# Optimization experiments

Hardware: AMD Instinct MI355X
Metric: run time of the kernel (lower is better)

The kernel has to match this reference:

```python
import jax, jax.numpy as jnp
import numpy as np

B, N, E, H = 4, 4096, 1024, 16
D = E // H


def setup_inputs() -> dict:
    key = jax.random.key(0)
    ks = jax.random.split(key, 8)
    s = 1.0 / np.sqrt(E)
    x = jax.random.normal(ks[0], (B, N, E), dtype=jnp.float32)
    # binary multiplicative sparsity pattern over the head-head score matrix
    sparsity_pattern = jax.random.randint(ks[1], (H, H), 0, 2).astype(jnp.float32)
    Wq = jax.random.normal(ks[2], (E, E), dtype=jnp.float32) * s
    bq = jax.random.normal(ks[3], (E,), dtype=jnp.float32) * s
    Wk = jax.random.normal(ks[4], (E, E), dtype=jnp.float32) * s
    bk = jax.random.normal(ks[5], (E,), dtype=jnp.float32) * s
    Wv = jax.random.normal(ks[6], (E, E), dtype=jnp.float32) * s
    bv = jax.random.normal(ks[7], (E,), dtype=jnp.float32) * s
    return {"x": x, "sparsity_pattern": sparsity_pattern,
            "Wq": Wq, "bq": bq, "Wk": Wk, "bk": bk, "Wv": Wv, "bv": bv}


def reference(x, sparsity_pattern, Wq, bq, Wk, bk, Wv, bv):
    b, n, e = x.shape
    # torch Linear: y = x @ W.T + b
    q = (x @ Wq.T + bq).reshape(b, n, H, D)
    k = (x @ Wk.T + bk).reshape(b, n, H, D)
    v = (x @ Wv.T + bv).reshape(b, n, H, D)
    # torch.matmul over last two dims of [B,N,H,D]: scores are [B,N,H,H]
    scores = jnp.einsum('bnhd,bngd->bnhg', q, k) * sparsity_pattern
    attn = jax.nn.softmax(scores, axis=-1)
    out = jnp.einsum('bnhg,bngd->bnhd', attn, v).reshape(b, n, e)
    return out
```

## Files before the change

kernel.cpp:

```cpp
#include <hip/hip_runtime.h>
#include <hip/hip_bf16.h>

#define M_   16384
#define K_   1024
#define NQKV 3072

typedef _Float16 f16x4 __attribute__((ext_vector_type(4)));
typedef _Float16 f16x8 __attribute__((ext_vector_type(8)));
typedef float    f32x4 __attribute__((ext_vector_type(4)));

__global__ __launch_bounds__(256) void cvt_f32_f16(const float* __restrict__ in,
                                                   _Float16* __restrict__ o, int n4) {
  int i = blockIdx.x * blockDim.x + threadIdx.x;
  const int stride = gridDim.x * blockDim.x;
  for (; i < n4; i += stride) {
    float4 v = ((const float4*)in)[i];
    f16x4 h; h[0] = (_Float16)v.x; h[1] = (_Float16)v.y;
    h[2] = (_Float16)v.z; h[3] = (_Float16)v.w;
    *(f16x4*)&o[(size_t)i * 4] = h;
  }
}

__global__ __launch_bounds__(256) void cvt3_f32_f16(
    const float* __restrict__ a, const float* __restrict__ b,
    const float* __restrict__ c, _Float16* __restrict__ o, int n4each) {
  const float* src = (blockIdx.y == 0) ? a : (blockIdx.y == 1) ? b : c;
  _Float16* dst = o + (size_t)blockIdx.y * n4each * 4;
  int i = blockIdx.x * blockDim.x + threadIdx.x;
  const int stride = gridDim.x * blockDim.x;
  for (; i < n4each; i += stride) {
    float4 v = ((const float4*)src)[i];
    f16x4 h; h[0] = (_Float16)v.x; h[1] = (_Float16)v.y;
    h[2] = (_Float16)v.z; h[3] = (_Float16)v.w;
    *(f16x4*)&dst[(size_t)i * 4] = h;
  }
}

__global__ __launch_bounds__(512, 2) void gemm_qkv(
    const _Float16* __restrict__ xh, const _Float16* __restrict__ wh,
    const float* __restrict__ bq, const float* __restrict__ bk,
    const float* __restrict__ bv, _Float16* __restrict__ qkv)
{
  __shared__ __align__(16) _Float16 As[2][256 * 64];
  __shared__ __align__(16) _Float16 Bs[2][256 * 64];

  const int tid  = threadIdx.x;
  const int ln   = tid & 63;
  const int w    = tid >> 6;
  const int wm2  = w >> 2;
  const int wn4  = w & 3;
  const int lcol = ln & 15, quad = ln >> 4;

  const int bid = blockIdx.x;
  const int swz = (bid & 7) * 96 + (bid >> 3);
  const int m0 = (swz / 12) * 256;
  const int n0 = (swz % 12) * 256;

  f32x4 acc[8][4];
#pragma unroll
  for (int i = 0; i < 8; ++i)
#pragma unroll
    for (int j = 0; j < 4; ++j) acc[i][j] = f32x4{0.f, 0.f, 0.f, 0.f};

  f16x8 a0[4][2], a1[4][2], b0[2][2], b1[2][2];

#define STAGE_A(BUF, KT, X)                                                    \
  { _Pragma("unroll")                                                          \
    for (int j = 0; j < 2; ++j) {                                              \
      const int c   = j * 512 + tid;                                           \
      const int rr  = c >> 3;                                                  \
      const int r   = (X) * 64 + (rr & 63) + ((rr >> 6) << 7);                 \
      const int cb  = (c & 7) ^ (r & 7);                                       \
      const int rr0 = j * 64 + w * 8;                                          \
      const int r0  = (X) * 64 + (rr0 & 63) + ((rr0 >> 6) << 7);               \
      __builtin_amdgcn_global_load_lds(                                        \
          (const __attribute__((address_space(1))) void*)(                     \
              xh + (size_t)(m0 + r) * K_ + (KT) * 64 + cb * 8),                \
          (__attribute__((address_space(3))) void*)(&As[BUF][r0 * 64]),        \
          16, 0, 0);                                                           \
    } }

#define STAGE_B(BUF, KT, Y)                                                    \
  { _Pragma("unroll")                                                          \
    for (int j = 0; j < 2; ++j) {                                              \
      const int c   = j * 512 + tid;                                           \
      const int rr  = c >> 3;                                                  \
      const int r   = ((rr >> 5) << 6) + (Y) * 32 + (rr & 31);                 \
      const int cb  = (c & 7) ^ (r & 7);                                       \
      const int rr0 = j * 64 + w * 8;                                          \
      const int r0  = ((rr0 >> 5) << 6) + (Y) * 32 + (rr0 & 31);               \
      __builtin_amdgcn_global_load_lds(                                        \
          (const __attribute__((address_space(1))) void*)(                     \
              wh + (size_t)(n0 + r) * K_ + (KT) * 64 + cb * 8),                \
          (__attribute__((address_space(3))) void*)(&Bs[BUF][r0 * 64]),        \
          16, 0, 0);                                                           \
    } }

#define RDA(DST, BUF, MH, KB)                                                  \
  _Pragma("unroll")                                                            \
  for (int mi = 0; mi < 4; ++mi) {                                             \
    const int ar = wm2 * 128 + (MH) * 64 + mi * 16 + lcol;                     \
    const int sw = ar & 7;                                                     \
    DST[mi][KB] = *(const f16x8*)&As[BUF][ar * 64 + (((KB)*4 + quad) ^ sw) * 8]; \
  }

#define RDB(DST, BUF, NH, KB)                                                  \
  _Pragma("unroll")                                                            \
  for (int ni = 0; ni < 2; ++ni) {                                             \
    const int br = wn4 * 64 + (NH) * 32 + ni * 16 + lcol;                      \
    const int sw = br & 7;                                                     \
    DST[ni][KB] = *(const f16x8*)&Bs[BUF][br * 64 + (((KB)*4 + quad) ^ sw) * 8]; \
  }

#define MFMA8(AARR, BARR, MH, NH, KB)                                          \
  __builtin_amdgcn_s_setprio(1);                                               \
  _Pragma("unroll")                                                            \
  for (int mi = 0; mi < 4; ++mi)                                               \
    _Pragma("unroll")                                                          \
    for (int ni = 0; ni < 2; ++ni)                                             \
      acc[(MH) * 4 + mi][(NH) * 2 + ni] =                                      \
          __builtin_amdgcn_mfma_f32_16x16x32_f16(                              \
              AARR[mi][KB], BARR[ni][KB], acc[(MH) * 4 + mi][(NH) * 2 + ni],   \
              0, 0, 0);                                                        \
  __builtin_amdgcn_s_setprio(0);

#define SB()    __builtin_amdgcn_sched_barrier(0)
#define BAR()   { __builtin_amdgcn_s_barrier(); SB(); }
#define LGKM(N) { asm volatile("s_waitcnt lgkmcnt(" #N ")" ::: "memory"); SB(); }
#define VM6()   asm volatile("s_waitcnt vmcnt(6)" ::: "memory")
#define VM0()   asm volatile("s_waitcnt vmcnt(0)" ::: "memory")

#define KTILE(BUF, STG1, STG2, STG3, STG4, WAIT4)                              \
  {                                               \
    RDB(b0, BUF, 0, 0); RDA(a0, BUF, 0, 0); SB();                              \
    RDB(b0, BUF, 0, 1); RDA(a0, BUF, 0, 1); SB();                              \
    STG1;                                                                      \
    BAR(); LGKM(6);  MFMA8(a0, b0, 0, 0, 0);                                   \
           LGKM(0);  MFMA8(a0, b0, 0, 0, 1); BAR();                            \
                                                        \
    RDA(a1, BUF, 1, 0); SB(); RDA(a1, BUF, 1, 1); SB();                        \
    STG2;                                                                      \
    BAR(); LGKM(4);  MFMA8(a1, b0, 1, 0, 0);                                   \
           LGKM(0);  MFMA8(a1, b0, 1, 0, 1); BAR();                            \
                                                        \
    RDB(b1, BUF, 1, 0); SB(); RDB(b1, BUF, 1, 1); SB();                        \
    STG3;                                                                      \
    BAR(); LGKM(2);  MFMA8(a1, b1, 1, 1, 0);                                   \
           LGKM(0);  MFMA8(a1, b1, 1, 1, 1); BAR();                            \
                                                 \
    STG4; WAIT4;                                                               \
    BAR();           MFMA8(a0, b1, 0, 1, 0);                                   \
                     MFMA8(a0, b1, 0, 1, 1); BAR();                            \
  }

  STAGE_A(0, 0, 0); STAGE_B(0, 0, 0); STAGE_A(0, 0, 1); STAGE_B(0, 0, 1);
  STAGE_B(1, 1, 0); STAGE_A(1, 1, 1); STAGE_B(1, 1, 1);
  VM6(); BAR();

#pragma unroll 1
  for (int it = 0; it < 7; ++it) {
    const int kt = it * 2;
    KTILE(0, STAGE_A(1, kt + 1, 0), STAGE_B(0, kt + 2, 0),
             STAGE_A(0, kt + 2, 1), STAGE_B(0, kt + 2, 1), VM6());
    KTILE(1, STAGE_A(0, kt + 2, 0), STAGE_B(1, kt + 3, 0),
             STAGE_A(1, kt + 3, 1), STAGE_B(1, kt + 3, 1), VM6());
  }
  KTILE(0, STAGE_A(1, 15, 0), , , , VM0());
  KTILE(1, , , , , );

#pragma unroll
  for (int nh = 0; nh < 4; ++nh) {
    const int col = n0 + wn4 * 64 + nh * 16 + lcol;
    const int seg = col >> 10, cs = col & 1023;
    const float bi = ((seg == 0) ? bq : (seg == 1) ? bk : bv)[cs];
#pragma unroll
    for (int mi = 0; mi < 8; ++mi) {
      const int r0 = m0 + wm2 * 128 + mi * 16 + quad * 4;
#pragma unroll
      for (int r = 0; r < 4; ++r)
        qkv[(size_t)(r0 + r) * 3072 + col] = (_Float16)(acc[mi][nh][r] + bi);
    }
  }
#undef STAGE_A
#undef STAGE_B
#undef RDA
#undef RDB
#undef MFMA8
#undef SB
#undef BAR
#undef LGKM
#undef VM6
#undef VM0
#undef KTILE
}

__global__ __launch_bounds__(256) void attn_kernel(
    const _Float16* __restrict__ qkv,
    const float* __restrict__ pat,
    float* __restrict__ out)
{
  __shared__ __align__(16) _Float16 Ps[4][16 * 24];
  __shared__ __align__(16) _Float16 Vt[4][64 * 24];

  const int tid  = threadIdx.x;
  const int ln   = tid & 63;
  const int wv   = tid >> 6;
  const int lcol = ln & 15, quad = ln >> 4;
  const int t    = blockIdx.x * 4 + wv;

  const _Float16* qg = qkv + (size_t)t * 3072;
  const _Float16* kg = qg + 1024;
  const _Float16* vg = qg + 2048;

  f16x8 vc[2];
  vc[0] = *(const f16x8*)(vg + ((ln >> 3)    ) * 64 + (ln & 7) * 8);
  vc[1] = *(const f16x8*)(vg + ((ln >> 3) + 8) * 64 + (ln & 7) * 8);
  f16x8 aq0 = *(const f16x8*)(qg + lcol * 64 + quad * 8);
  f16x8 aq1 = *(const f16x8*)(qg + lcol * 64 + 32 + quad * 8);
  f16x8 bk0 = *(const f16x8*)(kg + lcol * 64 + quad * 8);
  f16x8 bk1 = *(const f16x8*)(kg + lcol * 64 + 32 + quad * 8);
  float p4[4];
#pragma unroll
  for (int r = 0; r < 4; r++) p4[r] = pat[(quad * 4 + r) * 16 + lcol];

#pragma unroll
  for (int i = 0; i < 2; i++) {
    const int g = (ln >> 3) + i * 8, c = (ln & 7) * 8;
#pragma unroll
    for (int j = 0; j < 8; j++) Vt[wv][(c + j) * 24 + g] = vc[i][j];
  }

  f32x4 s = {0.f, 0.f, 0.f, 0.f};
  s = __builtin_amdgcn_mfma_f32_16x16x32_f16(aq0, bk0, s, 0, 0, 0);
  s = __builtin_amdgcn_mfma_f32_16x16x32_f16(aq1, bk1, s, 0, 0, 0);

#pragma unroll
  for (int r = 0; r < 4; r++) {
    const float sv = s[r] * p4[r];
    float m = sv;
#pragma unroll
    for (int msk = 1; msk < 16; msk <<= 1) m = fmaxf(m, __shfl_xor(m, msk, 64));
    const float e = __expf(sv - m);
    float su = e;
#pragma unroll
    for (int msk = 1; msk < 16; msk <<= 1) su += __shfl_xor(su, msk, 64);
    Ps[wv][(quad * 4 + r) * 24 + lcol] = (_Float16)(e / su);
  }

  f16x4 ap = *(const f16x4*)&Ps[wv][lcol * 24 + quad * 4];

  f32x4 o[4];
#pragma unroll
  for (int dt = 0; dt < 4; dt++) {
    f16x4 bvf = *(const f16x4*)&Vt[wv][(dt * 16 + lcol) * 24 + quad * 4];
    f32x4 z = {0.f, 0.f, 0.f, 0.f};
    o[dt] = __builtin_amdgcn_mfma_f32_16x16x16f16(ap, bvf, z, 0, 0, 0);
  }

  float* op = out + (size_t)t * 1024;
#pragma unroll
  for (int dt = 0; dt < 4; dt++)
#pragma unroll
    for (int r = 0; r < 4; r++)
      op[(quad * 4 + r) * 64 + dt * 16 + lcol] = o[dt][r];
}

extern "C" void kernel_launch(void* const* d_in, const int* in_sizes, int n_in,
                              void* d_out, int out_size, void* d_ws, size_t ws_size,
                              hipStream_t stream) {
  const float* x   = (const float*)d_in[0];
  const float* pat = (const float*)d_in[1];
  const float* Wq  = (const float*)d_in[2];
  const float* bq  = (const float*)d_in[3];
  const float* Wk  = (const float*)d_in[4];
  const float* bk  = (const float*)d_in[5];
  const float* Wv  = (const float*)d_in[6];
  const float* bv  = (const float*)d_in[7];

  _Float16* qkvh = (_Float16*)d_ws;
  _Float16* xh   = qkvh + (size_t)50331648;
  _Float16* wh   = qkvh + (size_t)67108864;

  cvt_f32_f16<<<4096, 256, 0, stream>>>(x, xh, 4194304);
  cvt3_f32_f16<<<dim3(256, 3), 256, 0, stream>>>(Wq, Wk, Wv, wh, 262144);

  gemm_qkv<<<768, 512, 0, stream>>>(xh, wh, bq, bk, bv, qkvh);
  attn_kernel<<<M_ / 4, 256, 0, stream>>>(qkvh, pat, (float*)d_out);
}
```

Baseline: 271.9 us.

## Restructure QKV GEMM K-loop into two-phase pipeline with register prefetch

Rewrites the K-tile schedule of the fused QKV projection GEMM. Each tile is now two phases with one barrier each, where there were four barrier-bracketed quadrants. The next tile's whole A/B stage is issued at the start of each tile, and the next tile's a0/b0 fragments are prefetched into registers (b0 ping-pongs between b0e/b0o) while the current MFMAs run. The aim is fewer barriers and better overlap of LDS reads with MFMA work. The cost is more live registers and a shallower global prefetch depth: it now runs one tile ahead and waits for vmcnt(0) each tile, so global latency may be less well hidden.

```diff
diff --git a/kernel.cpp b/kernel.cpp
--- a/kernel.cpp
+++ b/kernel.cpp
@@ -62,7 +62,7 @@
 #pragma unroll
     for (int j = 0; j < 4; ++j) acc[i][j] = f32x4{0.f, 0.f, 0.f, 0.f};
 
-  f16x8 a0[4][2], a1[4][2], b0[2][2], b1[2][2];
+  f16x8 a0[4][2], a1[4][2], b0e[2][2], b0o[2][2], b1[2][2];
 
 #define STAGE_A(BUF, KT, X)                                                    \
   { _Pragma("unroll")                                                          \
@@ -96,77 +96,79 @@
           16, 0, 0);                                                           \
     } }
 
-#define RDA(DST, BUF, MH, KB)                                                  \
+#define RDA(DST, BUF, MH)                                                      \
   _Pragma("unroll")                                                            \
   for (int mi = 0; mi < 4; ++mi) {                                             \
     const int ar = wm2 * 128 + (MH) * 64 + mi * 16 + lcol;                     \
     const int sw = ar & 7;                                                     \
-    DST[mi][KB] = *(const f16x8*)&As[BUF][ar * 64 + (((KB)*4 + quad) ^ sw) * 8]; \
-  }
-
-#define RDB(DST, BUF, NH, KB)                                                  \
+    DST[mi][0] = *(const f16x8*)&As[BUF][ar * 64 + ((quad    ) ^ sw) * 8];     \
+    DST[mi][1] = *(const f16x8*)&As[BUF][ar * 64 + ((quad + 4) ^ sw) * 8];     \
+  }
+
+#define RDB(DST, BUF, NH)                                                      \
   _Pragma("unroll")                                                            \
   for (int ni = 0; ni < 2; ++ni) {                                             \
     const int br = wn4 * 64 + (NH) * 32 + ni * 16 + lcol;                      \
     const int sw = br & 7;                                                     \
-    DST[ni][KB] = *(const f16x8*)&Bs[BUF][br * 64 + (((KB)*4 + quad) ^ sw) * 8]; \
-  }
-
-#define MFMA8(AARR, BARR, MH, NH, KB)                                          \
+    DST[ni][0] = *(const f16x8*)&Bs[BUF][br * 64 + ((quad    ) ^ sw) * 8];     \
+    DST[ni][1] = *(const f16x8*)&Bs[BUF][br * 64 + ((quad + 4) ^ sw) * 8];     \
+  }
+
+#define MFMA16(AARR, BARR, MH, NH)                                             \
   __builtin_amdgcn_s_setprio(1);                                               \
   _Pragma("unroll")                                                            \
-  for (int mi = 0; mi < 4; ++mi)                                               \
+  for (int kb = 0; kb < 2; ++kb)                                               \
     _Pragma("unroll")                                                          \
-    for (int ni = 0; ni < 2; ++ni)                                             \
-      acc[(MH) * 4 + mi][(NH) * 2 + ni] =                                      \
-          __builtin_amdgcn_mfma_f32_16x16x32_f16(                              \
-              AARR[mi][KB], BARR[ni][KB], acc[(MH) * 4 + mi][(NH) * 2 + ni],   \
-              0, 0, 0);                                                        \
+    for (int mi = 0; mi < 4; ++mi)                                             \
+      _Pragma("unroll")                                                        \
+      for (int ni = 0; ni < 2; ++ni)                                           \
+        acc[(MH) * 4 + mi][(NH) * 2 + ni] =                                    \
+            __builtin_amdgcn_mfma_f32_16x16x32_f16(                            \
+                AARR[mi][kb], BARR[ni][kb], acc[(MH) * 4 + mi][(NH) * 2 + ni], \
+                0, 0, 0);                                                      \
   __builtin_amdgcn_s_setprio(0);
 
 #define SB()    __builtin_amdgcn_sched_barrier(0)
 #define BAR()   { __builtin_amdgcn_s_barrier(); SB(); }
 #define LGKM(N) { asm volatile("s_waitcnt lgkmcnt(" #N ")" ::: "memory"); SB(); }
-#define VM6()   asm volatile("s_waitcnt vmcnt(6)" ::: "memory")
-#define VM0()   asm volatile("s_waitcnt vmcnt(0)" ::: "memory")
-
-#define KTILE(BUF, STG1, STG2, STG3, STG4, WAIT4)                              \
-  {                                               \
-    RDB(b0, BUF, 0, 0); RDA(a0, BUF, 0, 0); SB();                              \
-    RDB(b0, BUF, 0, 1); RDA(a0, BUF, 0, 1); SB();                              \
-    STG1;                                                                      \
-    BAR(); LGKM(6);  MFMA8(a0, b0, 0, 0, 0);                                   \
-           LGKM(0);  MFMA8(a0, b0, 0, 0, 1); BAR();                            \
-                                                        \
-    RDA(a1, BUF, 1, 0); SB(); RDA(a1, BUF, 1, 1); SB();                        \
-    STG2;                                                                      \
-    BAR(); LGKM(4);  MFMA8(a1, b0, 1, 0, 0);                                   \
-           LGKM(0);  MFMA8(a1, b0, 1, 0, 1); BAR();                            \
-                                                        \
-    RDB(b1, BUF, 1, 0); SB(); RDB(b1, BUF, 1, 1); SB();                        \
-    STG3;                                                                      \
-    BAR(); LGKM(2);  MFMA8(a1, b1, 1, 1, 0);                                   \
-           LGKM(0);  MFMA8(a1, b1, 1, 1, 1); BAR();                            \
-                                                 \
-    STG4; WAIT4;                                                               \
-    BAR();           MFMA8(a0, b1, 0, 1, 0);                                   \
-                     MFMA8(a0, b1, 0, 1, 1); BAR();                            \
+#define VM4()   { asm volatile("s_waitcnt vmcnt(4)" ::: "memory"); SB(); }
+#define VM0()   { asm volatile("s_waitcnt vmcnt(0)" ::: "memory"); SB(); }
+
+#define KTILE(CUR, B0C, B0N, T, NOTLAST)                                       \
+  {                            \
+    RDB(b1, CUR, 1); SB();                                                     \
+    if (NOTLAST) {                                                             \
+      STAGE_A(1 - (CUR), (T) + 1, 0); STAGE_B(1 - (CUR), (T) + 1, 0);          \
+      STAGE_A(1 - (CUR), (T) + 1, 1); STAGE_B(1 - (CUR), (T) + 1, 1);          \
+      SB();                                                                    \
+    }                                                                          \
+    LGKM(4);  MFMA16(a0, B0C, 0, 0);                                           \
+    RDA(a1, CUR, 1); SB();                                                     \
+    LGKM(8);  MFMA16(a0, b1, 0, 1);                                            \
+    if (NOTLAST) VM4();                                                        \
+    BAR();                                                                     \
+        \
+    if (NOTLAST) { RDA(a0, 1 - (CUR), 0); SB(); LGKM(8); }                     \
+    else         { LGKM(0); }                                                  \
+    MFMA16(a1, b1, 1, 1);                                                      \
+    if (NOTLAST) { RDB(B0N, 1 - (CUR), 0); SB(); LGKM(4); }                    \
+    else         { LGKM(0); }                                                  \
+    MFMA16(a1, B0C, 1, 0);                                                     \
+    if (NOTLAST) VM0();                                                        \
+    BAR();                                                                     \
   }
 
   STAGE_A(0, 0, 0); STAGE_B(0, 0, 0); STAGE_A(0, 0, 1); STAGE_B(0, 0, 1);
-  STAGE_B(1, 1, 0); STAGE_A(1, 1, 1); STAGE_B(1, 1, 1);
-  VM6(); BAR();
+  VM0(); BAR();
+  RDA(a0, 0, 0); SB(); RDB(b0e, 0, 0); SB();
 
 #pragma unroll 1
   for (int it = 0; it < 7; ++it) {
-    const int kt = it * 2;
-    KTILE(0, STAGE_A(1, kt + 1, 0), STAGE_B(0, kt + 2, 0),
-             STAGE_A(0, kt + 2, 1), STAGE_B(0, kt + 2, 1), VM6());
-    KTILE(1, STAGE_A(0, kt + 2, 0), STAGE_B(1, kt + 3, 0),
-             STAGE_A(1, kt + 3, 1), STAGE_B(1, kt + 3, 1), VM6());
-  }
-  KTILE(0, STAGE_A(1, 15, 0), , , , VM0());
-  KTILE(1, , , , , );
+    KTILE(0, b0e, b0o, it * 2,     1);
+    KTILE(1, b0o, b0e, it * 2 + 1, 1);
+  }
+  KTILE(0, b0e, b0o, 14, 1);
+  KTILE(1, b0o, b0e, 15, 0);
 
 #pragma unroll
   for (int nh = 0; nh < 4; ++nh) {
@@ -185,11 +187,11 @@
 #undef STAGE_B
 #undef RDA
 #undef RDB
-#undef MFMA8
+#undef MFMA16
 #undef SB
 #undef BAR
 #undef LGKM
-#undef VM6
+#undef VM4
 #undef VM0
 #undef KTILE
 }
```

Result: slower. 319.6 us (+17.5%).
